# Performance work log

Hardware: AMD Instinct MI355X
Metric: run time of the kernel (lower is better)

Reference implementation:

```python
import jax, jax.numpy as jnp
import numpy as np

BINS = 256

def _conv_x(t, k):
    # t: [N,1,H,W], k: [3] tap filter along width, 'same' padding
    return jax.lax.conv_general_dilated(t, k.reshape(1, 1, 1, 3), (1, 1), [(0, 0), (1, 1)])

def _conv_y(t, k):
    # t: [N,1,H,W], k: [3] tap filter along height, 'same' padding
    return jax.lax.conv_general_dilated(t, k.reshape(1, 1, 3, 1), (1, 1), [(1, 1), (0, 0)])

def calc_invCR(x):
    # Vectorized equivalent of the per-slice torch.histc loop:
    # 256-bin histogram over [-1,1] per (batch*channel) slice, Shannon entropy in bits / 8.
    n, _, h, w = x.shape
    res = h * w
    xf = x.reshape(n, res)
    valid = ((xf >= -1.0) & (xf <= 1.0)).astype(jnp.float32)
    # bin index; value exactly == max (1.0) falls into the last bin, matching torch.histc
    bins = jnp.clip(jnp.floor((xf + 1.0) * (BINS / 2.0)), 0, BINS - 1).astype(jnp.int32)
    counts = jnp.zeros((n, BINS), jnp.float32).at[jnp.arange(n)[:, None], bins].add(valid)
    p = counts / res
    ent = jnp.sum(jnp.where(p > 0, -p * jnp.log2(jnp.where(p > 0, p, 1.0)), 0.0))
    return ent / (8.0 * n)

def _forward(x, px, ux, cx, rx, py, uy, cy, ry):
    b, c, h, w = x.shape
    img = x.reshape(b * c, 1, h, w)
    cur = img
    xos, yos = [], []
    for lvl in range(5):
        xe, xo = cur[:, :, :, ::2], cur[:, :, :, 1::2]
        xo = xo - _conv_x(xe, px)
        xe = xe + _conv_x(xo, ux)
        xo = xo - _conv_x(xe, cx)
        xe = xe + _conv_x(xo, rx)
        ye, yo = xe[:, :, ::2, :], xe[:, :, 1::2, :]
        yo = yo - _conv_y(ye, py)
        if lvl < 2:
            ye = ye + _conv_y(yo, uy)
        # levels 3-5 in the source apply update_y to the (discarded) x?e tensor
        # (`x3e = x3e + self.update_y(x3o)`); that result is never used, so it is a
        # no-op for the output and is faithfully omitted here.
        yo = yo - _conv_y(ye, cy)
        ye = ye + _conv_y(yo, ry)
        xos.append(xo)
        yos.append(yo)
        cur = ye
    out = cur
    for xo, yo in zip(reversed(xos), reversed(yos)):
        out = jnp.concatenate((jnp.concatenate((out, yo), axis=2), xo), axis=3)
    deltas = jnp.fmod(out + 1.0, 2.0) - 1.0  # wrap residuals into [-1,1]
    loss1 = 255.0 * jnp.sqrt(jnp.mean(jnp.square(deltas)))
    loss0 = 255.0 * jnp.sqrt(jnp.mean(jnp.square(img)))
    invCR0 = calc_invCR(img)
    invCR1 = calc_invCR(deltas)
    return loss1, loss0, invCR0, invCR1

def setup_inputs() -> dict:
    key = jax.random.key(0)
    ks = jax.random.split(key, 9)
    inp = {"x": jax.random.uniform(ks[0], (32, 3, 512, 512), jnp.float32)}
    for i, name in enumerate(["px", "ux", "cx", "rx", "py", "uy", "cy", "ry"]):
        inp[name] = 0.25 * jax.random.normal(ks[i + 1], (3,), jnp.float32)
    return inp

def reference(x, px, ux, cx, rx, py, uy, cy, ry):
    return _forward(x, px, ux, cx, rx, py, uy, cy, ry)
```

## Files before the change

### kernel.cpp

```cpp
#include <hip/hip_runtime.h>
#include <math.h>

#define NIMG 96
#define NSLOT 1024
#define RES_INV (1.0f / 262144.0f)

__device__ __forceinline__ float wrap1(float v) {
  float t = v + 1.0f;
  return t - 2.0f * truncf(t * 0.5f) - 1.0f;
}
__device__ __forceinline__ int bin_fast(float v) {
  int b = (int)fmaf(v, 128.0f, 128.0f);
  return (b > 255) ? 255 : b;
}

template<int P, int DO_IMG>
__global__ void __launch_bounds__(256) kx(
    const float* __restrict__ src, float* __restrict__ xe_out,
    const float* __restrict__ kpx, const float* __restrict__ kux,
    const float* __restrict__ kcx, const float* __restrict__ krx,
    double* __restrict__ partial,
    unsigned* __restrict__ hist_img, unsigned* __restrict__ hist_delta)
{
  constexpr int W2 = 64 * P;
  constexpr int H  = 128 * P;
  __shared__ unsigned shd[2][257];
  __shared__ unsigned shi[2][257];

  const int t = threadIdx.x, w = t >> 6, lane = t & 63;
  const int hsel = w >> 1;
  const int img = blockIdx.y;
  const int r0 = blockIdx.x * 16 + w * 4;

  for (int i = t; i < 2 * 257; i += 256) ((unsigned*)shd)[i] = 0;
  if (DO_IMG)
    for (int i = t; i < 2 * 257; i += 256) ((unsigned*)shi)[i] = 0;
  __syncthreads();

  const float px0 = kpx[0], px1 = kpx[1], px2 = kpx[2];
  const float ux0 = kux[0], ux1 = kux[1], ux2 = kux[2];
  const float cx0 = kcx[0], cx1 = kcx[1], cx2 = kcx[2];
  const float rx0 = krx[0], rx1 = krx[1], rx2 = krx[2];

  const float* ip = src + (size_t)img * H * (2 * W2);
  float sqi = 0.f, sqd = 0.f;

  auto stepm = [&](float (&d)[P], float (&s)[P], float k0, float k1, float k2) {
    float L = __shfl_up(s[P - 1], 1); if (lane == 0) L = 0.f;
    float R = __shfl_down(s[0], 1);   if (lane == 63) R = 0.f;
    float prev = L;
#pragma unroll
    for (int j = 0; j < P; j++) {
      float nxt = (j == P - 1) ? R : s[(j + 1) < P ? (j + 1) : 0];
      d[j] = fmaf(k0, prev, fmaf(k1, s[j], fmaf(k2, nxt, d[j])));
      prev = s[j];
    }
  };

  float4 A[4], B[4];
#pragma unroll
  for (int j = 0; j < 4; ++j) {
    const float* rp = ip + (size_t)(r0 + j) * (2 * W2) + lane * (2 * P);
    if (P == 1) { float2 v = *(const float2*)rp; A[j].x = v.x; A[j].y = v.y; }
    else {
      A[j] = *(const float4*)rp;
      if (P == 4) B[j] = *(const float4*)(rp + 4);
    }
  }

#pragma unroll
  for (int j = 0; j < 4; ++j) {
    float e[P], o[P];
    e[0] = A[j].x; o[0] = A[j].y;
    if (P >= 2) { e[P > 1 ? 1 : 0] = A[j].z; o[P > 1 ? 1 : 0] = A[j].w; }
    if (P == 4) {
      e[P > 2 ? 2 : 0] = B[j].x; o[P > 2 ? 2 : 0] = B[j].y;
      e[P > 3 ? 3 : 0] = B[j].z; o[P > 3 ? 3 : 0] = B[j].w;
    }
    if (DO_IMG) {
#pragma unroll
      for (int jj = 0; jj < P; jj++) {
        sqi += e[jj] * e[jj] + o[jj] * o[jj];
        atomicAdd(&shi[hsel][bin_fast(e[jj])], 1u);
        atomicAdd(&shi[hsel][bin_fast(o[jj])], 1u);
      }
    }
    stepm(o, e, -px0, -px1, -px2);
    stepm(e, o,  ux0,  ux1,  ux2);
    stepm(o, e, -cx0, -cx1, -cx2);
    stepm(e, o,  rx0,  rx1,  rx2);
    float* orow = xe_out + ((size_t)img * H + r0 + j) * W2;
    if (P == 4) {
      *(float4*)(orow + lane * 4) =
          make_float4(e[0], e[P > 1 ? 1 : 0], e[P > 2 ? 2 : 0], e[P > 3 ? 3 : 0]);
    } else if (P == 2) {
      *(float2*)(orow + lane * 2) = make_float2(e[0], e[P > 1 ? 1 : 0]);
    } else {
      orow[lane] = e[0];
    }
#pragma unroll
    for (int jj = 0; jj < P; jj++) {
      float d = wrap1(o[jj]);
      sqd += d * d;
      atomicAdd(&shd[hsel][bin_fast(d)], 1u);
    }
  }

  for (int off = 32; off; off >>= 1) {
    sqd += __shfl_down(sqd, off);
    if (DO_IMG) sqi += __shfl_down(sqi, off);
  }
  if (lane == 0) {
    const int bid = blockIdx.x + blockIdx.y * gridDim.x;
    const int slot = (bid * 4 + w) & (NSLOT - 1);
    atomicAdd(&partial[NSLOT + slot], (double)sqd);
    if (DO_IMG) atomicAdd(&partial[slot], (double)sqi);
  }
  __syncthreads();
  unsigned hd = shd[0][t] + shd[1][t];
  if (hd) atomicAdd(&hist_delta[img * 256 + t], hd);
  if (DO_IMG) {
    unsigned hi = shi[0][t] + shi[1][t];
    if (hi) atomicAdd(&hist_img[img * 256 + t], hi);
  }
}

template<int P, int USE_UY>
__global__ void __launch_bounds__(256) ky(
    const float* __restrict__ xe, float* __restrict__ ye_out,
    const float* __restrict__ kpy, const float* __restrict__ kuy,
    const float* __restrict__ kcy, const float* __restrict__ kry,
    double* __restrict__ partial, unsigned* __restrict__ hist_delta)
{
  constexpr int W2 = 64 * P;
  constexpr int H2 = W2;
  constexpr int NSP = 256 / W2;
  constexpr int SEG = 16, WIN = 24;
  __shared__ unsigned shd[2][257];

  const int t = threadIdx.x;
  const int img = blockIdx.y;
  const int col = t % W2;
  const int half = t / W2;
  const int r0 = (blockIdx.x * NSP + half) * SEG;
  const int hsel = (t >> 7) & 1;

  for (int i = t; i < 2 * 257; i += 256) ((unsigned*)shd)[i] = 0;
  __syncthreads();

  const float py0 = kpy[0], py1 = kpy[1], py2 = kpy[2];
  const float uy0 = kuy[0], uy1 = kuy[1], uy2 = kuy[2];
  const float cy0 = kcy[0], cy1 = kcy[1], cy2 = kcy[2];
  const float ry0 = kry[0], ry1 = kry[1], ry2 = kry[2];

  const float* xin = xe + (size_t)img * (2 * H2) * W2 + col;
  float ee[WIN], oo[WIN];
#pragma unroll
  for (int q = 0; q < WIN; ++q) {
    const int g = r0 + q - 4;
    const int gc = (g < 0) ? 0 : ((g >= H2) ? (H2 - 1) : g);
    float v0 = xin[(size_t)(2 * gc) * W2];
    float v1 = xin[(size_t)(2 * gc) * W2 + W2];
    const bool ok = (unsigned)g < (unsigned)H2;
    ee[q] = ok ? v0 : 0.f;
    oo[q] = ok ? v1 : 0.f;
  }
#pragma unroll
  for (int q = 0; q < WIN; ++q) {
    float U = (q > 0) ? ee[q - 1] : 0.f;
    float D = (q < WIN - 1) ? ee[q + 1] : 0.f;
    oo[q] = fmaf(-py0, U, fmaf(-py1, ee[q], fmaf(-py2, D, oo[q])));
  }
  if (USE_UY) {
#pragma unroll
    for (int q = 0; q < WIN; ++q) {
      float U = (q > 0) ? oo[q - 1] : 0.f;
      float D = (q < WIN - 1) ? oo[q + 1] : 0.f;
      ee[q] = fmaf(uy0, U, fmaf(uy1, oo[q], fmaf(uy2, D, ee[q])));
    }
  }
#pragma unroll
  for (int q = 0; q < WIN; ++q) {
    float U = (q > 0) ? ee[q - 1] : 0.f;
    float D = (q < WIN - 1) ? ee[q + 1] : 0.f;
    oo[q] = fmaf(-cy0, U, fmaf(-cy1, ee[q], fmaf(-cy2, D, oo[q])));
  }
#pragma unroll
  for (int q = 0; q < WIN; ++q) {
    float U = (q > 0) ? oo[q - 1] : 0.f;
    float D = (q < WIN - 1) ? oo[q + 1] : 0.f;
    ee[q] = fmaf(ry0, U, fmaf(ry1, oo[q], fmaf(ry2, D, ee[q])));
  }

  float sqd = 0.f;
  float* outp = ye_out + (size_t)img * H2 * W2 + col;
#pragma unroll
  for (int q = 4; q < 4 + SEG; ++q) {
    const int g = r0 + q - 4;
    float d = wrap1(oo[q]);
    sqd += d * d;
    atomicAdd(&shd[hsel][bin_fast(d)], 1u);
    outp[(size_t)g * W2] = ee[q];
  }

  for (int off = 32; off; off >>= 1) sqd += __shfl_down(sqd, off);
  if ((t & 63) == 0) {
    const int bid = blockIdx.x + blockIdx.y * gridDim.x;
    atomicAdd(&partial[NSLOT + ((bid * 4 + (t >> 6)) & (NSLOT - 1))], (double)sqd);
  }
  __syncthreads();
  unsigned hd = shd[0][t] + shd[1][t];
  if (hd) atomicAdd(&hist_delta[img * 256 + t], hd);
}

__global__ void __launch_bounds__(256) klift_tail64(
    const float* __restrict__ src,
    const float* __restrict__ kpx, const float* __restrict__ kux,
    const float* __restrict__ kcx, const float* __restrict__ krx,
    const float* __restrict__ kpy, const float* __restrict__ kcy,
    const float* __restrict__ kry,
    double* __restrict__ partial, unsigned* __restrict__ hist_delta)
{
  __shared__ float tile[64][65];
  __shared__ unsigned shd[2][257];
  const int t = threadIdx.x;
  const int img = blockIdx.x;
  const int cd = t & 1;
  for (int i = t; i < 2 * 257; i += 256) ((unsigned*)shd)[i] = 0;

  const float* sp = src + (size_t)img * 64 * 64;
  for (int idx = t; idx < 64 * 16; idx += 256) {
    const int r = idx >> 4, c4 = (idx & 15) << 2;
    float4 v = *(const float4*)(sp + r * 64 + c4);
    tile[r][c4] = v.x; tile[r][c4 + 1] = v.y;
    tile[r][c4 + 2] = v.z; tile[r][c4 + 3] = v.w;
  }
  const float px0 = kpx[0], px1 = kpx[1], px2 = kpx[2];
  const float ux0 = kux[0], ux1 = kux[1], ux2 = kux[2];
  const float cx0 = kcx[0], cx1 = kcx[1], cx2 = kcx[2];
  const float rx0 = krx[0], rx1 = krx[1], rx2 = krx[2];
  const float pc0 = kpy[0] + kcy[0], pc1 = kpy[1] + kcy[1], pc2 = kpy[2] + kcy[2];
  const float ry0 = kry[0], ry1 = kry[1], ry2 = kry[2];
  float sqd = 0.f;
  __syncthreads();

  for (int l = 0; l < 2; ++l) {
    const int s = 1 << l, n = 64 >> l, half = n >> 1;
    const int totx = n * half;

    for (int idx = t; idx < totx; idx += 256) {
      const int r = (idx / half) * s, c = idx % half;
      float L = (c > 0) ? tile[r][(2 * c - 2) * s] : 0.f;
      float M = tile[r][2 * c * s];
      float R = (c < half - 1) ? tile[r][(2 * c + 2) * s] : 0.f;
      tile[r][(2 * c + 1) * s] -= px0 * L + px1 * M + px2 * R;
    }
    __syncthreads();
    for (int idx = t; idx < totx; idx += 256) {
      const int r = (idx / half) * s, c = idx % half;
      float L = (c > 0) ? tile[r][(2 * c - 1) * s] : 0.f;
      float M = tile[r][(2 * c + 1) * s];
      float R = (c < half - 1) ? tile[r][(2 * c + 3) * s] : 0.f;
      tile[r][2 * c * s] += ux0 * L + ux1 * M + ux2 * R;
    }
    __syncthreads();
    for (int idx = t; idx < totx; idx += 256) {
      const int r = (idx / half) * s, c = idx % half;
      float L = (c > 0) ? tile[r][(2 * c - 2) * s] : 0.f;
      float M = tile[r][2 * c * s];
      float R = (c < half - 1) ? tile[r][(2 * c + 2) * s] : 0.f;
      tile[r][(2 * c + 1) * s] -= cx0 * L + cx1 * M + cx2 * R;
    }
    __syncthreads();
    for (int idx = t; idx < totx; idx += 256) {
      const int r = (idx / half) * s, c = idx % half;
      float L = (c > 0) ? tile[r][(2 * c - 1) * s] : 0.f;
      float M = tile[r][(2 * c + 1) * s];
      float R = (c < half - 1) ? tile[r][(2 * c + 3) * s] : 0.f;
      tile[r][2 * c * s] += rx0 * L + rx1 * M + rx2 * R;
    }
    __syncthreads();
    for (int idx = t; idx < totx; idx += 256) {
      const int r = (idx / half) * s, c = idx % half;
      float d = wrap1(tile[r][(2 * c + 1) * s]);
      sqd += d * d;
      atomicAdd(&shd[cd][bin_fast(d)], 1u);
    }
    const int toty = half * half;
    for (int idx = t; idx < toty; idx += 256) {
      const int r = idx / half, j = idx % half, col = j * 2 * s;
      float U = (r > 0) ? tile[(2 * r - 2) * s][col] : 0.f;
      float M = tile[(2 * r) * s][col];
      float D = (r < half - 1) ? tile[(2 * r + 2) * s][col] : 0.f;
      tile[(2 * r + 1) * s][col] -= pc0 * U + pc1 * M + pc2 * D;
    }
    __syncthreads();
    for (int idx = t; idx < toty; idx += 256) {
      const int r = idx / half, j = idx % half, col = j * 2 * s;
      float U = (r > 0) ? tile[(2 * r - 1) * s][col] : 0.f;
      float M = tile[(2 * r + 1) * s][col];
      float D = (r < half - 1) ? tile[(2 * r + 3) * s][col] : 0.f;
      tile[(2 * r) * s][col] += ry0 * U + ry1 * M + ry2 * D;
    }
    __syncthreads();
    for (int idx = t; idx < toty; idx += 256) {
      const int r = idx / half, j = idx % half, col = j * 2 * s;
      float d = wrap1(tile[(2 * r + 1) * s][col]);
      sqd += d * d;
      atomicAdd(&shd[cd][bin_fast(d)], 1u);
      if (l == 1) {
        float d2 = wrap1(tile[(2 * r) * s][col]);
        sqd += d2 * d2;
        atomicAdd(&shd[cd][bin_fast(d2)], 1u);
      }
    }
    __syncthreads();
  }

  for (int off = 32; off; off >>= 1) sqd += __shfl_down(sqd, off);
  __shared__ float swv[4];
  if ((t & 63) == 0) swv[t >> 6] = sqd;
  __syncthreads();
  if (t == 0) {
    double tot = (double)swv[0] + swv[1] + swv[2] + swv[3];
    atomicAdd(&partial[NSLOT + (img & (NSLOT - 1))], tot);
  }
  unsigned hd = shd[0][t] + shd[1][t];
  if (hd) atomicAdd(&hist_delta[img * 256 + t], hd);
}

__global__ void __launch_bounds__(256) kfinal(
    const double* __restrict__ partial,
    const unsigned* __restrict__ hist_img,
    const unsigned* __restrict__ hist_delta,
    float* __restrict__ out)
{
  __shared__ double sI[256], sD[256], sPi[256], sPd[256];
  const int t = threadIdx.x;
  double entI = 0.0, entD = 0.0;
  for (int img = 0; img < NIMG; ++img) {
    unsigned ci = hist_img[img * 256 + t];
    if (ci) { float p = (float)ci * RES_INV; entI += (double)(-p * log2f(p)); }
    unsigned cd = hist_delta[img * 256 + t];
    if (cd) { float p = (float)cd * RES_INV; entD += (double)(-p * log2f(p)); }
  }
  double pi = 0.0, pd = 0.0;
  for (int s = t; s < NSLOT; s += 256) {
    pi += partial[s];
    pd += partial[NSLOT + s];
  }
  sI[t] = entI; sD[t] = entD; sPi[t] = pi; sPd[t] = pd;
  __syncthreads();
  for (int s = 128; s; s >>= 1) {
    if (t < s) {
      sI[t] += sI[t + s]; sD[t] += sD[t + s];
      sPi[t] += sPi[t + s]; sPd[t] += sPd[t + s];
    }
    __syncthreads();
  }
  if (t == 0) {
    const double tot = (double)NIMG * 262144.0;
    out[0] = (float)(255.0 * sqrt(sPd[0] / tot));
    out[1] = (float)(255.0 * sqrt(sPi[0] / tot));
    out[2] = (float)(sI[0] / (8.0 * NIMG));
    out[3] = (float)(sD[0] / (8.0 * NIMG));
  }
}

extern "C" void kernel_launch(void* const* d_in, const int* in_sizes, int n_in,
                              void* d_out, int out_size, void* d_ws, size_t ws_size,
                              hipStream_t stream)
{
  const float* x  = (const float*)d_in[0];
  const float* px = (const float*)d_in[1];
  const float* ux = (const float*)d_in[2];
  const float* cx = (const float*)d_in[3];
  const float* rx = (const float*)d_in[4];
  const float* py = (const float*)d_in[5];
  const float* uy = (const float*)d_in[6];
  const float* cy = (const float*)d_in[7];
  const float* ry = (const float*)d_in[8];
  float* out = (float*)d_out;

  char* ws = (char*)d_ws;
  double*   partial    = (double*)ws;
  unsigned* hist_img   = (unsigned*)(ws + 2 * NSLOT * 8);
  unsigned* hist_delta = (unsigned*)(ws + 2 * NSLOT * 8 + NIMG * 256 * 4);
  float* bxe  = (float*)(ws + ((size_t)1 << 20));
  float* bye0 = (float*)(ws + ((size_t)50 << 20));
  float* bye1 = (float*)(ws + ((size_t)76 << 20));
  float* bye2 = (float*)(ws + ((size_t)83 << 20));

  hipMemsetAsync(ws, 0, 2 * NSLOT * 8 + 2 * NIMG * 256 * 4, stream);

  kx<4, 1><<<dim3(32, NIMG), 256, 0, stream>>>(
      x, bxe, px, ux, cx, rx, partial, hist_img, hist_delta);
  ky<4, 1><<<dim3(16, NIMG), 256, 0, stream>>>(
      bxe, bye0, py, uy, cy, ry, partial, hist_delta);
  kx<2, 0><<<dim3(16, NIMG), 256, 0, stream>>>(
      bye0, bxe, px, ux, cx, rx, partial, hist_img, hist_delta);
  ky<2, 1><<<dim3(4, NIMG), 256, 0, stream>>>(
      bxe, bye1, py, uy, cy, ry, partial, hist_delta);
  kx<1, 0><<<dim3(8, NIMG), 256, 0, stream>>>(
      bye1, bxe, px, ux, cx, rx, partial, hist_img, hist_delta);
  ky<1, 0><<<dim3(1, NIMG), 256, 0, stream>>>(
      bxe, bye2, py, uy, cy, ry, partial, hist_delta);
  klift_tail64<<<NIMG, 256, 0, stream>>>(bye2, px, ux, cx, rx, py, cy, ry,
                                         partial, hist_delta);
  kfinal<<<1, 256, 0, stream>>>(partial, hist_img, hist_delta, out);
}
```

Before: 98.64 us.

## Use per-thread byte histograms in LDS for the first horizontal lifting level

Adds a dedicated first-level horizontal lifting kernel in which each thread keeps private 8-bit histograms for the image and delta values in a large LDS buffer. This replaces the shared-memory atomic increments of the generic kernel, and the per-thread bins are merged at the end with packed-byte SWAR sums. Each block now handles 64 rows, with four wave-rows of input kept in flight as a software prefetch ring. The image-histogram path is removed from the generic template. The cost is about 132KB of LDS per block, which allows only one 256-thread block per CU and may reduce latency hiding on this memory-bound stage.

```diff
diff --git a/kernel.cpp b/kernel.cpp
--- a/kernel.cpp
+++ b/kernel.cpp
@@ -12,6 +12,116 @@
 __device__ __forceinline__ int bin_fast(float v) {
   int b = (int)fmaf(v, 128.0f, 128.0f);
   return (b > 255) ? 255 : b;
+}
+
+__global__ void __launch_bounds__(256, 1) kx4_bh(
+    const float* __restrict__ src, float* __restrict__ xe_out,
+    const float* __restrict__ kpx, const float* __restrict__ kux,
+    const float* __restrict__ kcx, const float* __restrict__ krx,
+    double* __restrict__ partial,
+    unsigned* __restrict__ hist_img, unsigned* __restrict__ hist_delta)
+{
+  constexpr int W2 = 256, H = 512;
+  constexpr int STRB = 516;
+  __shared__ unsigned char bh[256 * STRB];
+
+  const int t = threadIdx.x, w = t >> 6, lane = t & 63;
+  const int img = blockIdx.y;
+  const int r0 = blockIdx.x * 64 + w * 16;
+
+  unsigned* bw = (unsigned*)bh;
+  for (int i = t; i < 256 * (STRB / 4); i += 256) bw[i] = 0;
+  __syncthreads();
+
+  const float px0 = kpx[0], px1 = kpx[1], px2 = kpx[2];
+  const float ux0 = kux[0], ux1 = kux[1], ux2 = kux[2];
+  const float cx0 = kcx[0], cx1 = kcx[1], cx2 = kcx[2];
+  const float rx0 = krx[0], rx1 = krx[1], rx2 = krx[2];
+
+  const float* ip = src + (size_t)img * H * (2 * W2);
+  unsigned char* myh = &bh[t * STRB];
+  float sqi = 0.f, sqd = 0.f;
+
+  auto stepm = [&](float (&d)[4], float (&s)[4], float k0, float k1, float k2) {
+    float L = __shfl_up(s[3], 1); if (lane == 0) L = 0.f;
+    float R = __shfl_down(s[0], 1); if (lane == 63) R = 0.f;
+    float prev = L;
+#pragma unroll
+    for (int j = 0; j < 4; j++) {
+      float nxt = (j == 3) ? R : s[j + 1 < 4 ? j + 1 : 0];
+      d[j] = fmaf(k0, prev, fmaf(k1, s[j], fmaf(k2, nxt, d[j])));
+      prev = s[j];
+    }
+  };
+
+  float4 A[4], B[4];
+#pragma unroll
+  for (int j = 0; j < 4; ++j) {
+    const float* rp = ip + (size_t)(r0 + j) * (2 * W2) + lane * 8;
+    A[j] = *(const float4*)rp;
+    B[j] = *(const float4*)(rp + 4);
+  }
+
+  for (int r = 0; r < 16; ++r) {
+    const int cur = r & 3;
+    float e[4], o[4];
+    e[0] = A[cur].x; o[0] = A[cur].y; e[1] = A[cur].z; o[1] = A[cur].w;
+    e[2] = B[cur].x; o[2] = B[cur].y; e[3] = B[cur].z; o[3] = B[cur].w;
+    if (r + 4 < 16) {
+      const float* rp = ip + (size_t)(r0 + r + 4) * (2 * W2) + lane * 8;
+      A[cur] = *(const float4*)rp;
+      B[cur] = *(const float4*)(rp + 4);
+    }
+#pragma unroll
+    for (int j = 0; j < 4; j++) {
+      sqi += e[j] * e[j] + o[j] * o[j];
+      myh[bin_fast(e[j])]++;
+      myh[bin_fast(o[j])]++;
+    }
+    stepm(o, e, -px0, -px1, -px2);
+    stepm(e, o,  ux0,  ux1,  ux2);
+    stepm(o, e, -cx0, -cx1, -cx2);
+    stepm(e, o,  rx0,  rx1,  rx2);
+    float* orow = xe_out + ((size_t)img * H + r0 + r) * W2;
+    *(float4*)(orow + lane * 4) = make_float4(e[0], e[1], e[2], e[3]);
+#pragma unroll
+    for (int j = 0; j < 4; j++) {
+      float d = wrap1(o[j]);
+      sqd += d * d;
+      myh[256 + bin_fast(d)]++;
+    }
+  }
+
+  for (int off = 32; off; off >>= 1) {
+    sqd += __shfl_down(sqd, off);
+    sqi += __shfl_down(sqi, off);
+  }
+  if (lane == 0) {
+    const int bid = blockIdx.x + blockIdx.y * gridDim.x;
+    const int slot = (bid * 4 + w) & (NSLOT - 1);
+    atomicAdd(&partial[NSLOT + slot], (double)sqd);
+    atomicAdd(&partial[slot], (double)sqi);
+  }
+  __syncthreads();
+
+  {
+    const int h = t >> 7;
+    const int g = t & 127;
+    unsigned s0 = 0, s1 = 0;
+    for (int c = h * 128; c < h * 128 + 128; ++c) {
+      unsigned wv = bw[c * (STRB / 4) + g];
+      s0 += wv & 0x00FF00FFu;
+      s1 += (wv >> 8) & 0x00FF00FFu;
+    }
+    const unsigned b0 = s0 & 0xFFFFu, b2 = s0 >> 16;
+    const unsigned b1 = s1 & 0xFFFFu, b3 = s1 >> 16;
+    unsigned* dst = (g < 64) ? &hist_img[img * 256 + 4 * g]
+                             : &hist_delta[img * 256 + 4 * (g - 64)];
+    if (b0) atomicAdd(dst + 0, b0);
+    if (b1) atomicAdd(dst + 1, b1);
+    if (b2) atomicAdd(dst + 2, b2);
+    if (b3) atomicAdd(dst + 3, b3);
+  }
 }
 
 template<int P, int DO_IMG>
@@ -25,7 +135,6 @@
   constexpr int W2 = 64 * P;
   constexpr int H  = 128 * P;
   __shared__ unsigned shd[2][257];
-  __shared__ unsigned shi[2][257];
 
   const int t = threadIdx.x, w = t >> 6, lane = t & 63;
   const int hsel = w >> 1;
@@ -33,8 +142,6 @@
   const int r0 = blockIdx.x * 16 + w * 4;
 
   for (int i = t; i < 2 * 257; i += 256) ((unsigned*)shd)[i] = 0;
-  if (DO_IMG)
-    for (int i = t; i < 2 * 257; i += 256) ((unsigned*)shi)[i] = 0;
   __syncthreads();
 
   const float px0 = kpx[0], px1 = kpx[1], px2 = kpx[2];
@@ -43,7 +150,7 @@
   const float rx0 = krx[0], rx1 = krx[1], rx2 = krx[2];
 
   const float* ip = src + (size_t)img * H * (2 * W2);
-  float sqi = 0.f, sqd = 0.f;
+  float sqd = 0.f;
 
   auto stepm = [&](float (&d)[P], float (&s)[P], float k0, float k1, float k2) {
     float L = __shfl_up(s[P - 1], 1); if (lane == 0) L = 0.f;
@@ -76,14 +183,6 @@
     if (P == 4) {
       e[P > 2 ? 2 : 0] = B[j].x; o[P > 2 ? 2 : 0] = B[j].y;
       e[P > 3 ? 3 : 0] = B[j].z; o[P > 3 ? 3 : 0] = B[j].w;
-    }
-    if (DO_IMG) {
-#pragma unroll
-      for (int jj = 0; jj < P; jj++) {
-        sqi += e[jj] * e[jj] + o[jj] * o[jj];
-        atomicAdd(&shi[hsel][bin_fast(e[jj])], 1u);
-        atomicAdd(&shi[hsel][bin_fast(o[jj])], 1u);
-      }
     }
     stepm(o, e, -px0, -px1, -px2);
     stepm(e, o,  ux0,  ux1,  ux2);
@@ -106,23 +205,15 @@
     }
   }
 
-  for (int off = 32; off; off >>= 1) {
-    sqd += __shfl_down(sqd, off);
-    if (DO_IMG) sqi += __shfl_down(sqi, off);
-  }
+  for (int off = 32; off; off >>= 1) sqd += __shfl_down(sqd, off);
   if (lane == 0) {
     const int bid = blockIdx.x + blockIdx.y * gridDim.x;
     const int slot = (bid * 4 + w) & (NSLOT - 1);
     atomicAdd(&partial[NSLOT + slot], (double)sqd);
-    if (DO_IMG) atomicAdd(&partial[slot], (double)sqi);
   }
   __syncthreads();
   unsigned hd = shd[0][t] + shd[1][t];
   if (hd) atomicAdd(&hist_delta[img * 256 + t], hd);
-  if (DO_IMG) {
-    unsigned hi = shi[0][t] + shi[1][t];
-    if (hi) atomicAdd(&hist_img[img * 256 + t], hi);
-  }
 }
 
 template<int P, int USE_UY>
@@ -393,7 +484,7 @@
 
   hipMemsetAsync(ws, 0, 2 * NSLOT * 8 + 2 * NIMG * 256 * 4, stream);
 
-  kx<4, 1><<<dim3(32, NIMG), 256, 0, stream>>>(
+  kx4_bh<<<dim3(8, NIMG), 256, 0, stream>>>(
       x, bxe, px, ux, cx, rx, partial, hist_img, hist_delta);
   ky<4, 1><<<dim3(16, NIMG), 256, 0, stream>>>(
       bxe, bye0, py, uy, cy, ry, partial, hist_delta);
```

After: 181.9 us. +84.4%, slower.
